# Kernel tuning notes

Hardware: AMD Instinct MI355X
Metric: run time of the kernel (lower is better)

Reference implementation:

```python
import jax, jax.numpy as jnp
import numpy as np

DIM = 128
N = 4096


def setup_inputs() -> dict:
    key = jax.random.key(0)
    ks = jax.random.split(key, 12)
    d = DIM
    s = 0.02
    inp = jax.random.normal(ks[0], (N, 2 * d), dtype=jnp.float32)
    # H = myLinear: (2d -> 5d -> 1), tanh after each layer
    Hw1 = jax.random.normal(ks[1], (2 * d, 5 * d), dtype=jnp.float32) * s
    Hb1 = jax.random.normal(ks[2], (5 * d,), dtype=jnp.float32) * s
    Hw2 = jax.random.normal(ks[3], (5 * d, 1), dtype=jnp.float32) * s
    Hb2 = jax.random.normal(ks[4], (1,), dtype=jnp.float32) * s
    # augment_f: (d -> 4d -> 8d -> d*d), tanh after each layer
    Aw1 = jax.random.normal(ks[5], (d, 4 * d), dtype=jnp.float32) * s
    Ab1 = jax.random.normal(ks[6], (4 * d,), dtype=jnp.float32) * s
    Aw2 = jax.random.normal(ks[7], (4 * d, 8 * d), dtype=jnp.float32) * s
    Ab2 = jax.random.normal(ks[8], (8 * d,), dtype=jnp.float32) * s
    Aw3 = jax.random.normal(ks[9], (8 * d, d * d), dtype=jnp.float32) * s
    Ab3 = jax.random.normal(ks[10], (d * d,), dtype=jnp.float32) * s
    u = jax.random.uniform(ks[11], (d,), dtype=jnp.float32, minval=-0.001, maxval=0.001)
    return {"t": 0, "inp": inp, "Hw1": Hw1, "Hb1": Hb1, "Hw2": Hw2, "Hb2": Hb2,
            "Aw1": Aw1, "Ab1": Ab1, "Aw2": Aw2, "Ab2": Ab2, "Aw3": Aw3, "Ab3": Ab3, "u": u}


def reference(t, inp, Hw1, Hb1, Hw2, Hb2, Aw1, Ab1, Aw2, Ab2, Aw3, Ab3, u):
    d = DIM
    n = inp.shape[0]

    def H_scalar(z):  # z: [2d] -> scalar
        h = jnp.tanh(z @ Hw1 + Hb1)
        return jnp.tanh(h @ Hw2 + Hb2)[0]

    # per-sample gradient of scalar H w.r.t. input (== batch_jacobian squeeze)
    g = jax.vmap(jax.grad(H_scalar))(inp)  # [N, 2d]
    dx = g[:, :d]
    dv = -g[:, d:]

    x = inp[:, :d]
    h1 = jnp.tanh(x @ Aw1 + Ab1)            # [N, 4d]
    h2 = jnp.tanh(h1 @ Aw2 + Ab2)           # [N, 8d]
    gq = jnp.tanh(h2 @ Aw3 + Ab3).reshape(n, d, d)  # [N, d, d]
    dv = dv + jnp.einsum("nij,j->ni", gq, u)
    return jnp.concatenate([dx, dv], axis=-1)  # [N, 2d]
```

## Files before the change

### kernel.cpp

```cpp
#include <hip/hip_runtime.h>
#include <hip/hip_bf16.h>
#include <cstdint>


typedef __bf16 bf16_t;
typedef __bf16 bf16x4_t __attribute__((ext_vector_type(4)));
typedef __bf16 bf16x8_t __attribute__((ext_vector_type(8)));
typedef float f32x4_t __attribute__((ext_vector_type(4)));
typedef float f32x16_t __attribute__((ext_vector_type(16)));
typedef int intx4_t __attribute__((ext_vector_type(4)));
typedef int intx8_t __attribute__((ext_vector_type(8)));

#define DIMD 128
#define NROW 4096
#define SMEM_BYTES 18432

__device__ __forceinline__ float fast_tanh(float x) {
  float t = __builtin_amdgcn_exp2f(x * 2.8853900817779268f);
  return 1.f - 2.f * __builtin_amdgcn_rcpf(t + 1.f);
}

__device__ __forceinline__ uint8_t to_fp8(float x) {
  return (uint8_t)(__builtin_amdgcn_cvt_pk_fp8_f32(x, x, 0, false) & 0xff);
}

__device__ __forceinline__ void g2l16(const void* gp, void* lp) {
  __builtin_amdgcn_global_load_lds(
      reinterpret_cast<__attribute__((address_space(1))) void*>(
          reinterpret_cast<uintptr_t>(gp)),
      reinterpret_cast<__attribute__((address_space(3))) void*>(
          reinterpret_cast<uintptr_t>(lp)),
      16, 0, 0);
}

template <int EPI>
__device__ __forceinline__ void gemm_body(char* smem, int bx, int by,
                                          const bf16_t* A, int lda,
                                          const bf16_t* B, int ldb, int K,
                                          const float* bias, void* outp,
                                          int ldo) {
  constexpr int BK = 32;
  bf16_t* As = (bf16_t*)smem;
  bf16_t* Bs = As + 4096;

  const int m0 = bx * 128;
  const int n0 = by * 128;
  const int tid = threadIdx.x;
  const int wave = tid >> 6;
  const int lane = tid & 63;
  const int wm = wave >> 1;
  const int wn = wave & 1;

  const int sr = lane >> 2;
  const int sk = (((lane & 3) ^ ((sr >> 1) & 3)) * 8);
  const int fr = lane & 15;
  const int fk = (((lane >> 4) ^ ((fr >> 1) & 3)) * 8);

  f32x4_t acc[4][4] = {};

  for (int k0 = 0; k0 < K; k0 += BK) {
    if (k0) __syncthreads();
#pragma unroll
    for (int t = 0; t < 2; ++t) {
      const int rb = wave * 32 + t * 16;
      g2l16(A + (size_t)(m0 + rb + sr) * lda + (k0 + sk), As + rb * BK);
      g2l16(B + (size_t)(n0 + rb + sr) * ldb + (k0 + sk), Bs + rb * BK);
    }
    __syncthreads();

    bf16x8_t af[4], bb[4];
#pragma unroll
    for (int t = 0; t < 4; ++t) {
      af[t] = *(const bf16x8_t*)(As + (wm * 64 + t * 16 + fr) * BK + fk);
      bb[t] = *(const bf16x8_t*)(Bs + (wn * 64 + t * 16 + fr) * BK + fk);
    }
#pragma unroll
    for (int i = 0; i < 4; ++i)
#pragma unroll
      for (int j = 0; j < 4; ++j)
        acc[i][j] = __builtin_amdgcn_mfma_f32_16x16x32_bf16(af[i], bb[j],
                                                            acc[i][j], 0, 0, 0);
  }

  if constexpr (EPI == 0) {
    bf16_t* O = (bf16_t*)outp;
#pragma unroll
    for (int i = 0; i < 4; ++i) {
      const int row = m0 + wm * 64 + i * 16 + (lane >> 4) * 4;
#pragma unroll
      for (int j = 0; j < 4; ++j) {
        const int col = n0 + wn * 64 + j * 16 + fr;
        const float b = bias[col];
#pragma unroll
        for (int r = 0; r < 4; ++r)
          O[(size_t)(row + r) * ldo + col] = (bf16_t)fast_tanh(acc[i][j][r] + b);
      }
    }
  } else if constexpr (EPI == 1) {
    float* O = (float*)outp;
    const float sgn = (n0 >= DIMD) ? -1.f : 1.f;
#pragma unroll
    for (int i = 0; i < 4; ++i) {
      const int row = m0 + wm * 64 + i * 16 + (lane >> 4) * 4;
#pragma unroll
      for (int j = 0; j < 4; ++j) {
        const int col = n0 + wn * 64 + j * 16 + fr;
#pragma unroll
        for (int r = 0; r < 4; ++r)
          O[(size_t)(row + r) * ldo + col] = sgn * acc[i][j][r];
      }
    }
  } else {
    uint8_t* O = (uint8_t*)outp;
#pragma unroll
    for (int i = 0; i < 4; ++i) {
      const int row = m0 + wm * 64 + i * 16 + (lane >> 4) * 4;
#pragma unroll
      for (int j = 0; j < 4; ++j) {
        const int col = n0 + wn * 64 + j * 16 + fr;
        const float b = bias[col];
#pragma unroll
        for (int r = 0; r < 4; ++r)
          O[(size_t)(row + r) * ldo + col] =
              to_fp8(64.f * fast_tanh(acc[i][j][r] + b));
      }
    }
  }
}

__device__ __forceinline__ void a3_body(char* smem, int bx, int by,
                                        const uint8_t* A, const uint8_t* B,
                                        float* dvA, const float* ab3,
                                        const float* uvec) {
  constexpr int BK = 64, K = 1024;
  uint8_t* As = (uint8_t*)smem;
  uint8_t* Bs = As + 8192;
  float* red = (float*)(smem + 16384);
  float* us = red + 128;
  float* a3s = us + 128;

  const int m0 = bx * 128;
  const int n0 = by * 128;
  const int tid = threadIdx.x;
  const int wave = tid >> 6;
  const int lane = tid & 63;
  const int wm = wave >> 1;
  const int wn = wave & 1;

  if (tid < 128) {
    red[tid] = 0.f;
    us[tid] = uvec[tid];
    a3s[tid] = ab3[n0 + tid];
  }

  const int sr = lane >> 2;
  const int sk = ((lane & 3) ^ ((sr >> 1) & 3)) * 16;

  const int rl = lane & 31;
  const int w = (rl >> 1) & 3;
  const int c0 = lane >> 5;
  const int sLo = ((2 * c0) ^ w) * 16;
  const int sHi = ((2 * c0 + 1) ^ w) * 16;

  f32x16_t acc[2][2] = {};

  for (int k0 = 0; k0 < K; k0 += BK) {
    if (k0) __syncthreads();
#pragma unroll
    for (int t = 0; t < 2; ++t) {
      const int rb = t * 64 + wave * 16;
      g2l16(A + (size_t)(m0 + rb + sr) * K + (k0 + sk), As + rb * BK);
      g2l16(B + (size_t)(n0 + rb + sr) * K + (k0 + sk), Bs + rb * BK);
    }
    __syncthreads();

    intx8_t af[2], bf[2];
#pragma unroll
    for (int i = 0; i < 2; ++i) {
      const int ra = (wm * 64 + i * 32 + rl) * BK;
      intx4_t lo = *(const intx4_t*)(As + ra + sLo);
      intx4_t hi = *(const intx4_t*)(As + ra + sHi);
      af[i] = __builtin_shufflevector(lo, hi, 0, 1, 2, 3, 4, 5, 6, 7);
      const int rb2 = (wn * 64 + i * 32 + rl) * BK;
      intx4_t lob = *(const intx4_t*)(Bs + rb2 + sLo);
      intx4_t hib = *(const intx4_t*)(Bs + rb2 + sHi);
      bf[i] = __builtin_shufflevector(lob, hib, 0, 1, 2, 3, 4, 5, 6, 7);
    }
#pragma unroll
    for (int i = 0; i < 2; ++i)
#pragma unroll
      for (int j = 0; j < 2; ++j)
        acc[i][j] = __builtin_amdgcn_mfma_scale_f32_32x32x64_f8f6f4(
            af[i], bf[j], acc[i][j], 0, 0, 0, 0x79797979, 0, 0x79797979);
  }

  const int q = lane >> 5;
#pragma unroll
  for (int i = 0; i < 2; ++i) {
    float sums[16];
#pragma unroll
    for (int r = 0; r < 16; ++r) sums[r] = 0.f;
#pragma unroll
    for (int j = 0; j < 2; ++j) {
      const int c = wn * 64 + j * 32 + rl;
      const float uu = us[c];
      const float b3 = a3s[c];
#pragma unroll
      for (int r = 0; r < 16; ++r) sums[r] += fast_tanh(acc[i][j][r] + b3) * uu;
    }
#pragma unroll
    for (int d = 1; d < 32; d <<= 1)
#pragma unroll
      for (int r = 0; r < 16; ++r) sums[r] += __shfl_xor(sums[r], d, 64);
    if (rl == 0) {
      const int rowb = wm * 64 + i * 32 + 4 * q;
#pragma unroll
      for (int r = 0; r < 16; ++r)
        atomicAdd(&red[rowb + (r & 3) + 8 * (r >> 2)], sums[r]);
    }
  }
  __syncthreads();
  if (tid < 128) dvA[(size_t)(m0 + tid) * 128 + by] = red[tid];
}

__device__ __forceinline__ void tcvt_body(char* smem, const float* in,
                                          bf16_t* out, int R, int C, int bx,
                                          int by) {
  float(*t)[33] = (float(*)[33])smem;
  const int c0 = bx * 32;
  const int r0 = by * 32;
  const int tx = threadIdx.x & 31;
  const int ty = threadIdx.x >> 5;
#pragma unroll
  for (int k = 0; k < 4; ++k)
    t[ty + k * 8][tx] = in[(size_t)(r0 + ty + k * 8) * C + c0 + tx];
  __syncthreads();
#pragma unroll
  for (int k = 0; k < 4; ++k)
    out[(size_t)(c0 + ty + k * 8) * R + r0 + tx] = (bf16_t)t[tx][ty + k * 8];
}

__device__ __forceinline__ void aw3t_body(char* smem, const float* Aw3,
                                          uint8_t* Aw3T8, int b) {
  float(*t)[33] = (float(*)[33])smem;
  const int c0 = (b & 511) * 32;
  const int r0 = (b >> 9) * 32;
  const int tx = threadIdx.x & 31;
  const int ty = threadIdx.x >> 5;
#pragma unroll
  for (int k = 0; k < 4; ++k)
    t[ty + k * 8][tx] = Aw3[(size_t)(r0 + ty + k * 8) * 16384 + c0 + tx];
  __syncthreads();
#pragma unroll
  for (int k = 0; k < 4; ++k)
    Aw3T8[(size_t)(c0 + ty + k * 8) * 1024 + r0 + tx] =
        to_fp8(64.f * t[tx][ty + k * 8]);
}

__device__ __forceinline__ void hgrad_row(int row, const bf16_t* h,
                                          const float* Hw2, const float* Hb2,
                                          bf16_t* wout) {
  const int lane = threadIdx.x & 63;
  float hv[10], wv[10];
  float pre2 = 0.f;
#pragma unroll
  for (int t = 0; t < 10; ++t) {
    const int j = lane + t * 64;
    hv[t] = (float)h[(size_t)row * 640 + j];
    wv[t] = Hw2[j];
    pre2 += hv[t] * wv[t];
  }
#pragma unroll
  for (int d = 1; d < 64; d <<= 1) pre2 += __shfl_xor(pre2, d, 64);
  const float y = fast_tanh(pre2 + Hb2[0]);
  const float s = 1.f - y * y;
#pragma unroll
  for (int t = 0; t < 10; ++t) {
    const int j = lane + t * 64;
    wout[(size_t)row * 640 + j] = (bf16_t)(s * wv[t] * (1.f - hv[t] * hv[t]));
  }
}

__global__ __launch_bounds__(256) void prep_small(
    const float* __restrict__ inp, bf16_t* __restrict__ inp_bf,
    const float* __restrict__ Hw1, bf16_t* __restrict__ Hw1_bf,
    bf16_t* __restrict__ Hw1T, const float* __restrict__ Aw1,
    bf16_t* __restrict__ Aw1T, const float* __restrict__ Aw2,
    bf16_t* __restrict__ Aw2T) {
  __shared__ __align__(16) char smem[4224];
  int b = blockIdx.x;
  if (b < 1184) {
    const int i = b * 256 + threadIdx.x;
    const int na4 = NROW * 256 / 4;
    const float4* in;
    bf16x4_t* out;
    int j;
    if (i < na4) {
      in = (const float4*)inp; out = (bf16x4_t*)inp_bf; j = i;
    } else {
      j = i - na4;
      if (j >= 256 * 640 / 4) return;
      in = (const float4*)Hw1; out = (bf16x4_t*)Hw1_bf;
    }
    const float4 v = in[j];
    bf16x4_t o = {(bf16_t)v.x, (bf16_t)v.y, (bf16_t)v.z, (bf16_t)v.w};
    out[j] = o;
  } else {
    int s = b - 1184;
    if (s < 160) tcvt_body(smem, Hw1, Hw1T, 256, 640, s % 20, s / 20);
    else if (s < 224) { s -= 160; tcvt_body(smem, Aw1, Aw1T, 128, 512, s % 16, s / 16); }
    else { s -= 224; tcvt_body(smem, Aw2, Aw2T, 512, 1024, s % 32, s / 32); }
  }
}

__global__ __launch_bounds__(256) void launch1(
    const bf16_t* __restrict__ inp_bf, const bf16_t* __restrict__ Hw1T,
    const float* __restrict__ Hb1, bf16_t* __restrict__ h_bf,
    const bf16_t* __restrict__ Aw1T, const float* __restrict__ Ab1,
    bf16_t* __restrict__ h1_bf, const float* __restrict__ Aw3,
    uint8_t* __restrict__ Aw3T8) {
  __shared__ __align__(16) char smem[SMEM_BYTES];
  const int b = blockIdx.x;
  if (b < 160) {
    gemm_body<0>(smem, b % 32, b / 32, inp_bf, 256, Hw1T, 256, 256, Hb1, h_bf, 640);
  } else if (b < 288) {
    const int i = b - 160;
    gemm_body<0>(smem, i % 32, i / 32, inp_bf, 256, Aw1T, 128, 128, Ab1, h1_bf, 512);
  } else {
    aw3t_body(smem, Aw3, Aw3T8, b - 288);
  }
}

__global__ __launch_bounds__(256) void launch2(
    const bf16_t* __restrict__ h1_bf, const bf16_t* __restrict__ Aw2T,
    const float* __restrict__ Ab2, uint8_t* __restrict__ h2_f8,
    const bf16_t* __restrict__ h_bf, const float* __restrict__ Hw2,
    const float* __restrict__ Hb2, bf16_t* __restrict__ w_bf) {
  __shared__ __align__(16) char smem[SMEM_BYTES];
  const int b = blockIdx.x;
  if (b < 256) {
    gemm_body<3>(smem, b % 32, b / 32, h1_bf, 512, Aw2T, 512, 512, Ab2, h2_f8, 1024);
  } else {
    const int row = (b - 256) * 4 + (threadIdx.x >> 6);
    hgrad_row(row, h_bf, Hw2, Hb2, w_bf);
  }
}

__global__ __launch_bounds__(256) void launch3(
    const bf16_t* __restrict__ w_bf, const bf16_t* __restrict__ Hw1_bf,
    float* __restrict__ out, const uint8_t* __restrict__ h2_f8,
    const uint8_t* __restrict__ Aw3T8, float* __restrict__ dvA,
    const float* __restrict__ Ab3, const float* __restrict__ uvec) {
  __shared__ __align__(16) char smem[SMEM_BYTES];
  const int b = blockIdx.x;
  if (b < 64) {
    gemm_body<1>(smem, b % 32, b / 32, w_bf, 640, Hw1_bf, 640, 640, nullptr, out, 256);
  } else {
    const int i = b - 64;
    a3_body(smem, i & 31, i >> 5, h2_f8, Aw3T8, dvA, Ab3, uvec);
  }
}

__global__ __launch_bounds__(256) void combine(float* __restrict__ out,
                                               const float* __restrict__ dvA) {
  const int i = blockIdx.x * 256 + threadIdx.x;
  out[(size_t)(i >> 7) * 256 + 128 + (i & 127)] += dvA[i];
}

extern "C" void kernel_launch(void* const* d_in, const int* in_sizes, int n_in,
                              void* d_out, int out_size, void* d_ws,
                              size_t ws_size, hipStream_t stream) {
  (void)in_sizes; (void)n_in; (void)out_size; (void)ws_size;
  const float* inp = (const float*)d_in[1];
  const float* Hw1 = (const float*)d_in[2];
  const float* Hb1 = (const float*)d_in[3];
  const float* Hw2 = (const float*)d_in[4];
  const float* Hb2 = (const float*)d_in[5];
  const float* Aw1 = (const float*)d_in[6];
  const float* Ab1 = (const float*)d_in[7];
  const float* Aw2 = (const float*)d_in[8];
  const float* Ab2 = (const float*)d_in[9];
  const float* Aw3 = (const float*)d_in[10];
  const float* Ab3 = (const float*)d_in[11];
  const float* u = (const float*)d_in[12];
  float* out = (float*)d_out;

  char* ws = (char*)d_ws;
  bf16_t* inp_bf = (bf16_t*)ws;   ws += (size_t)NROW * 256 * 2;
  bf16_t* Hw1_bf = (bf16_t*)ws;   ws += (size_t)256 * 640 * 2;
  bf16_t* Hw1T = (bf16_t*)ws;     ws += (size_t)640 * 256 * 2;
  bf16_t* Aw1T = (bf16_t*)ws;     ws += (size_t)512 * 128 * 2;
  bf16_t* Aw2T = (bf16_t*)ws;     ws += (size_t)1024 * 512 * 2;
  uint8_t* Aw3T8 = (uint8_t*)ws;  ws += (size_t)16384 * 1024;
  bf16_t* h_bf = (bf16_t*)ws;     ws += (size_t)NROW * 640 * 2;
  bf16_t* w_bf = (bf16_t*)ws;     ws += (size_t)NROW * 640 * 2;
  bf16_t* h1_bf = (bf16_t*)ws;    ws += (size_t)NROW * 512 * 2;
  uint8_t* h2_f8 = (uint8_t*)ws;  ws += (size_t)NROW * 1024;
  float* dvA = (float*)ws;        ws += (size_t)NROW * 128 * 4;

  prep_small<<<1920, 256, 0, stream>>>(inp, inp_bf, Hw1, Hw1_bf, Hw1T, Aw1,
                                       Aw1T, Aw2, Aw2T);
  launch1<<<288 + 16384, 256, 0, stream>>>(inp_bf, Hw1T, Hb1, h_bf, Aw1T, Ab1,
                                           h1_bf, Aw3, Aw3T8);
  launch2<<<256 + 1024, 256, 0, stream>>>(h1_bf, Aw2T, Ab2, h2_f8, h_bf, Hw2,
                                          Hb2, w_bf);
  launch3<<<64 + 4096, 256, 0, stream>>>(w_bf, Hw1_bf, out, h2_f8, Aw3T8, dvA,
                                         Ab3, u);
  combine<<<2048, 256, 0, stream>>>(out, dvA);
}
```

Measured before the change: 265.2 us.

## Fuse combine via atomics, enlarge A3 tiles, rebalance prep work across launches

Drops the separate combine kernel and dvA buffer. The out tensor is zeroed inside launch2, the A3 reduction and the dv part of the H-gradient GEMM accumulate into it with atomicAdd, and only the dx part is written directly. The A3 GEMM tile grows to 256x128 so each block covers four N-subtiles, cutting the number of blocks. The Aw3 fp8 transpose is split between launch1 and launch2, the Aw2 transpose and Hw1 cast move from prep into launch1, and the transpose store is vectorized to uchar4. The atomics add contention and make the float summation order nondeterministic.

After: 252.9 us. -4.6%, faster.

```diff
diff --git a/kernel.cpp b/kernel.cpp
--- a/kernel.cpp
+++ b/kernel.cpp
@@ -14,6 +14,7 @@
 #define DIMD 128
 #define NROW 4096
 #define SMEM_BYTES 18432
+#define SMEM3_BYTES 26624
 
 __device__ __forceinline__ float fast_tanh(float x) {
   float t = __builtin_amdgcn_exp2f(x * 2.8853900817779268f);
@@ -98,7 +99,7 @@
     }
   } else if constexpr (EPI == 1) {
     float* O = (float*)outp;
-    const float sgn = (n0 >= DIMD) ? -1.f : 1.f;
+    const bool dx = (n0 < DIMD);
 #pragma unroll
     for (int i = 0; i < 4; ++i) {
       const int row = m0 + wm * 64 + i * 16 + (lane >> 4) * 4;
@@ -106,8 +107,11 @@
       for (int j = 0; j < 4; ++j) {
         const int col = n0 + wn * 64 + j * 16 + fr;
 #pragma unroll
-        for (int r = 0; r < 4; ++r)
-          O[(size_t)(row + r) * ldo + col] = sgn * acc[i][j][r];
+        for (int r = 0; r < 4; ++r) {
+          const size_t idx = (size_t)(row + r) * ldo + col;
+          if (dx) O[idx] = acc[i][j][r];
+          else atomicAdd(&O[idx], -acc[i][j][r]);
+        }
       }
     }
   } else {
@@ -130,25 +134,23 @@
 
 __device__ __forceinline__ void a3_body(char* smem, int bx, int by,
                                         const uint8_t* A, const uint8_t* B,
-                                        float* dvA, const float* ab3,
+                                        float* out, const float* ab3,
                                         const float* uvec) {
   constexpr int BK = 64, K = 1024;
   uint8_t* As = (uint8_t*)smem;
-  uint8_t* Bs = As + 8192;
-  float* red = (float*)(smem + 16384);
-  float* us = red + 128;
+  uint8_t* Bs = As + 16384;
+  float* red = (float*)(smem + 24576);
+  float* us = red + 256;
   float* a3s = us + 128;
 
-  const int m0 = bx * 128;
+  const int m0 = bx * 256;
   const int n0 = by * 128;
   const int tid = threadIdx.x;
   const int wave = tid >> 6;
   const int lane = tid & 63;
-  const int wm = wave >> 1;
-  const int wn = wave & 1;
-
+
+  red[tid] = 0.f;
   if (tid < 128) {
-    red[tid] = 0.f;
     us[tid] = uvec[tid];
     a3s[tid] = ab3[n0 + tid];
   }
@@ -162,36 +164,43 @@
   const int sLo = ((2 * c0) ^ w) * 16;
   const int sHi = ((2 * c0 + 1) ^ w) * 16;
 
-  f32x16_t acc[2][2] = {};
+  f32x16_t acc[2][4] = {};
 
   for (int k0 = 0; k0 < K; k0 += BK) {
     if (k0) __syncthreads();
 #pragma unroll
+    for (int t = 0; t < 4; ++t) {
+      const int rb = t * 64 + wave * 16;
+      g2l16(A + (size_t)(m0 + rb + sr) * K + (k0 + sk), As + rb * BK);
+    }
+#pragma unroll
     for (int t = 0; t < 2; ++t) {
       const int rb = t * 64 + wave * 16;
-      g2l16(A + (size_t)(m0 + rb + sr) * K + (k0 + sk), As + rb * BK);
       g2l16(B + (size_t)(n0 + rb + sr) * K + (k0 + sk), Bs + rb * BK);
     }
     __syncthreads();
 
-    intx8_t af[2], bf[2];
+    intx8_t af[2], bfr[4];
 #pragma unroll
     for (int i = 0; i < 2; ++i) {
-      const int ra = (wm * 64 + i * 32 + rl) * BK;
+      const int ra = (wave * 64 + i * 32 + rl) * BK;
       intx4_t lo = *(const intx4_t*)(As + ra + sLo);
       intx4_t hi = *(const intx4_t*)(As + ra + sHi);
       af[i] = __builtin_shufflevector(lo, hi, 0, 1, 2, 3, 4, 5, 6, 7);
-      const int rb2 = (wn * 64 + i * 32 + rl) * BK;
+    }
+#pragma unroll
+    for (int j = 0; j < 4; ++j) {
+      const int rb2 = (j * 32 + rl) * BK;
       intx4_t lob = *(const intx4_t*)(Bs + rb2 + sLo);
       intx4_t hib = *(const intx4_t*)(Bs + rb2 + sHi);
-      bf[i] = __builtin_shufflevector(lob, hib, 0, 1, 2, 3, 4, 5, 6, 7);
+      bfr[j] = __builtin_shufflevector(lob, hib, 0, 1, 2, 3, 4, 5, 6, 7);
     }
 #pragma unroll
     for (int i = 0; i < 2; ++i)
 #pragma unroll
-      for (int j = 0; j < 2; ++j)
+      for (int j = 0; j < 4; ++j)
         acc[i][j] = __builtin_amdgcn_mfma_scale_f32_32x32x64_f8f6f4(
-            af[i], bf[j], acc[i][j], 0, 0, 0, 0x79797979, 0, 0x79797979);
+            af[i], bfr[j], acc[i][j], 0, 0, 0, 0x79797979, 0, 0x79797979);
   }
 
   const int q = lane >> 5;
@@ -201,8 +210,8 @@
 #pragma unroll
     for (int r = 0; r < 16; ++r) sums[r] = 0.f;
 #pragma unroll
-    for (int j = 0; j < 2; ++j) {
-      const int c = wn * 64 + j * 32 + rl;
+    for (int j = 0; j < 4; ++j) {
+      const int c = j * 32 + rl;
       const float uu = us[c];
       const float b3 = a3s[c];
 #pragma unroll
@@ -213,14 +222,14 @@
 #pragma unroll
       for (int r = 0; r < 16; ++r) sums[r] += __shfl_xor(sums[r], d, 64);
     if (rl == 0) {
-      const int rowb = wm * 64 + i * 32 + 4 * q;
+      const int rowb = wave * 64 + i * 32 + 4 * q;
 #pragma unroll
       for (int r = 0; r < 16; ++r)
         atomicAdd(&red[rowb + (r & 3) + 8 * (r >> 2)], sums[r]);
     }
   }
   __syncthreads();
-  if (tid < 128) dvA[(size_t)(m0 + tid) * 128 + by] = red[tid];
+  atomicAdd(&out[(size_t)(m0 + tid) * 256 + 128 + by], red[tid]);
 }
 
 __device__ __forceinline__ void tcvt_body(char* smem, const float* in,
@@ -251,10 +260,14 @@
   for (int k = 0; k < 4; ++k)
     t[ty + k * 8][tx] = Aw3[(size_t)(r0 + ty + k * 8) * 16384 + c0 + tx];
   __syncthreads();
-#pragma unroll
-  for (int k = 0; k < 4; ++k)
-    Aw3T8[(size_t)(c0 + ty + k * 8) * 1024 + r0 + tx] =
-        to_fp8(64.f * t[tx][ty + k * 8]);
+  const int cl = threadIdx.x >> 3;
+  const int j = (threadIdx.x & 7) * 4;
+  uchar4 v;
+  v.x = to_fp8(64.f * t[j + 0][cl]);
+  v.y = to_fp8(64.f * t[j + 1][cl]);
+  v.z = to_fp8(64.f * t[j + 2][cl]);
+  v.w = to_fp8(64.f * t[j + 3][cl]);
+  *(uchar4*)(Aw3T8 + (size_t)(c0 + cl) * 1024 + r0 + j) = v;
 }
 
 __device__ __forceinline__ void hgrad_row(int row, const bf16_t* h,
@@ -281,35 +294,23 @@
   }
 }
 
-__global__ __launch_bounds__(256) void prep_small(
+__global__ __launch_bounds__(256) void launch0(
     const float* __restrict__ inp, bf16_t* __restrict__ inp_bf,
-    const float* __restrict__ Hw1, bf16_t* __restrict__ Hw1_bf,
-    bf16_t* __restrict__ Hw1T, const float* __restrict__ Aw1,
-    bf16_t* __restrict__ Aw1T, const float* __restrict__ Aw2,
-    bf16_t* __restrict__ Aw2T) {
+    const float* __restrict__ Hw1, bf16_t* __restrict__ Hw1T,
+    const float* __restrict__ Aw1, bf16_t* __restrict__ Aw1T) {
   __shared__ __align__(16) char smem[4224];
   int b = blockIdx.x;
-  if (b < 1184) {
+  if (b < 1024) {
     const int i = b * 256 + threadIdx.x;
-    const int na4 = NROW * 256 / 4;
-    const float4* in;
-    bf16x4_t* out;
-    int j;
-    if (i < na4) {
-      in = (const float4*)inp; out = (bf16x4_t*)inp_bf; j = i;
-    } else {
-      j = i - na4;
-      if (j >= 256 * 640 / 4) return;
-      in = (const float4*)Hw1; out = (bf16x4_t*)Hw1_bf;
-    }
-    const float4 v = in[j];
+    const float4 v = ((const float4*)inp)[i];
     bf16x4_t o = {(bf16_t)v.x, (bf16_t)v.y, (bf16_t)v.z, (bf16_t)v.w};
-    out[j] = o;
+    ((bf16x4_t*)inp_bf)[i] = o;
+  } else if (b < 1184) {
+    int s = b - 1024;
+    tcvt_body(smem, Hw1, Hw1T, 256, 640, s % 20, s / 20);
   } else {
     int s = b - 1184;
-    if (s < 160) tcvt_body(smem, Hw1, Hw1T, 256, 640, s % 20, s / 20);
-    else if (s < 224) { s -= 160; tcvt_body(smem, Aw1, Aw1T, 128, 512, s % 16, s / 16); }
-    else { s -= 224; tcvt_body(smem, Aw2, Aw2T, 512, 1024, s % 32, s / 32); }
+    tcvt_body(smem, Aw1, Aw1T, 128, 512, s % 16, s / 16);
   }
 }
 
@@ -317,7 +318,9 @@
     const bf16_t* __restrict__ inp_bf, const bf16_t* __restrict__ Hw1T,
     const float* __restrict__ Hb1, bf16_t* __restrict__ h_bf,
     const bf16_t* __restrict__ Aw1T, const float* __restrict__ Ab1,
-    bf16_t* __restrict__ h1_bf, const float* __restrict__ Aw3,
+    bf16_t* __restrict__ h1_bf, const float* __restrict__ Aw2,
+    bf16_t* __restrict__ Aw2T, const float* __restrict__ Hw1,
+    bf16_t* __restrict__ Hw1_bf, const float* __restrict__ Aw3,
     uint8_t* __restrict__ Aw3T8) {
   __shared__ __align__(16) char smem[SMEM_BYTES];
   const int b = blockIdx.x;
@@ -326,8 +329,16 @@
   } else if (b < 288) {
     const int i = b - 160;
     gemm_body<0>(smem, i % 32, i / 32, inp_bf, 256, Aw1T, 128, 128, Ab1, h1_bf, 512);
+  } else if (b < 800) {
+    const int s = b - 288;
+    tcvt_body(smem, Aw2, Aw2T, 512, 1024, s % 32, s / 32);
+  } else if (b < 960) {
+    const int i = (b - 800) * 256 + threadIdx.x;
+    const float4 v = ((const float4*)Hw1)[i];
+    bf16x4_t o = {(bf16_t)v.x, (bf16_t)v.y, (bf16_t)v.z, (bf16_t)v.w};
+    ((bf16x4_t*)Hw1_bf)[i] = o;
   } else {
-    aw3t_body(smem, Aw3, Aw3T8, b - 288);
+    aw3t_body(smem, Aw3, Aw3T8, b - 960);
   }
 }
 
@@ -335,36 +346,37 @@
     const bf16_t* __restrict__ h1_bf, const bf16_t* __restrict__ Aw2T,
     const float* __restrict__ Ab2, uint8_t* __restrict__ h2_f8,
     const bf16_t* __restrict__ h_bf, const float* __restrict__ Hw2,
-    const float* __restrict__ Hb2, bf16_t* __restrict__ w_bf) {
+    const float* __restrict__ Hb2, bf16_t* __restrict__ w_bf,
+    float* __restrict__ out, const float* __restrict__ Aw3,
+    uint8_t* __restrict__ Aw3T8) {
   __shared__ __align__(16) char smem[SMEM_BYTES];
   const int b = blockIdx.x;
   if (b < 256) {
     gemm_body<3>(smem, b % 32, b / 32, h1_bf, 512, Aw2T, 512, 512, Ab2, h2_f8, 1024);
-  } else {
+  } else if (b < 1280) {
     const int row = (b - 256) * 4 + (threadIdx.x >> 6);
     hgrad_row(row, h_bf, Hw2, Hb2, w_bf);
+  } else if (b < 2304) {
+    const int i = (b - 1280) * 256 + threadIdx.x;
+    ((float4*)out)[i] = make_float4(0.f, 0.f, 0.f, 0.f);
+  } else {
+    aw3t_body(smem, Aw3, Aw3T8, 8192 + (b - 2304));
   }
 }
 
 __global__ __launch_bounds__(256) void launch3(
     const bf16_t* __restrict__ w_bf, const bf16_t* __restrict__ Hw1_bf,
     float* __restrict__ out, const uint8_t* __restrict__ h2_f8,
-    const uint8_t* __restrict__ Aw3T8, float* __restrict__ dvA,
-    const float* __restrict__ Ab3, const float* __restrict__ uvec) {
-  __shared__ __align__(16) char smem[SMEM_BYTES];
+    const uint8_t* __restrict__ Aw3T8, const float* __restrict__ Ab3,
+    const float* __restrict__ uvec) {
+  __shared__ __align__(16) char smem[SMEM3_BYTES];
   const int b = blockIdx.x;
   if (b < 64) {
     gemm_body<1>(smem, b % 32, b / 32, w_bf, 640, Hw1_bf, 640, 640, nullptr, out, 256);
   } else {
     const int i = b - 64;
-    a3_body(smem, i & 31, i >> 5, h2_f8, Aw3T8, dvA, Ab3, uvec);
-  }
-}
-
-__global__ __launch_bounds__(256) void combine(float* __restrict__ out,
-                                               const float* __restrict__ dvA) {
-  const int i = blockIdx.x * 256 + threadIdx.x;
-  out[(size_t)(i >> 7) * 256 + 128 + (i & 127)] += dvA[i];
+    a3_body(smem, i & 15, i >> 4, h2_f8, Aw3T8, out, Ab3, uvec);
+  }
 }
 
 extern "C" void kernel_launch(void* const* d_in, const int* in_sizes, int n_in,
@@ -396,15 +408,11 @@
   bf16_t* w_bf = (bf16_t*)ws;     ws += (size_t)NROW * 640 * 2;
   bf16_t* h1_bf = (bf16_t*)ws;    ws += (size_t)NROW * 512 * 2;
   uint8_t* h2_f8 = (uint8_t*)ws;  ws += (size_t)NROW * 1024;
-  float* dvA = (float*)ws;        ws += (size_t)NROW * 128 * 4;
-
-  prep_small<<<1920, 256, 0, stream>>>(inp, inp_bf, Hw1, Hw1_bf, Hw1T, Aw1,
-                                       Aw1T, Aw2, Aw2T);
-  launch1<<<288 + 16384, 256, 0, stream>>>(inp_bf, Hw1T, Hb1, h_bf, Aw1T, Ab1,
-                                           h1_bf, Aw3, Aw3T8);
-  launch2<<<256 + 1024, 256, 0, stream>>>(h1_bf, Aw2T, Ab2, h2_f8, h_bf, Hw2,
-                                          Hb2, w_bf);
-  launch3<<<64 + 4096, 256, 0, stream>>>(w_bf, Hw1_bf, out, h2_f8, Aw3T8, dvA,
-                                         Ab3, u);
-  combine<<<2048, 256, 0, stream>>>(out, dvA);
-}
+
+  launch0<<<1248, 256, 0, stream>>>(inp, inp_bf, Hw1, Hw1T, Aw1, Aw1T);
+  launch1<<<9152, 256, 0, stream>>>(inp_bf, Hw1T, Hb1, h_bf, Aw1T, Ab1, h1_bf,
+                                    Aw2, Aw2T, Hw1, Hw1_bf, Aw3, Aw3T8);
+  launch2<<<10496, 256, 0, stream>>>(h1_bf, Aw2T, Ab2, h2_f8, h_bf, Hw2, Hb2,
+                                     w_bf, out, Aw3, Aw3T8);
+  launch3<<<2112, 256, 0, stream>>>(w_bf, Hw1_bf, out, h2_f8, Aw3T8, Ab3, u);
+}
```
